# Kernel optimization log

Hardware: AMD Instinct MI355X
Metric: run time of the kernel (lower is better)

Reference implementation:

```python
import jax, jax.numpy as jnp
import numpy as np

N_USERS = 50000
N_ENT = 100000
N_EDGES = 2_000_000
N_INTER = 1_000_000
CHANNEL = 64
N_HEADS = 2
D_K = CHANNEL // N_HEADS
N_HOPS = 2
N_REL = 10  # relation_emb has N_REL-1 rows


def setup_inputs() -> dict:
    key = jax.random.key(0)
    ks = jax.random.split(key, 8)
    user_emb = jax.random.normal(ks[0], (N_USERS, CHANNEL), jnp.float32) * 0.1
    entity_emb = jax.random.normal(ks[1], (N_ENT, CHANNEL), jnp.float32) * 0.1
    relation_emb = jax.random.normal(ks[2], (N_REL - 1, CHANNEL), jnp.float32) * 0.1
    W_Q = jax.random.normal(ks[3], (CHANNEL, CHANNEL), jnp.float32) * (1.0 / np.sqrt(CHANNEL))
    edge_index = jax.random.randint(ks[4], (2, N_EDGES), 0, N_ENT)
    edge_type = jax.random.randint(ks[5], (N_EDGES,), 1, N_REL)  # in [1, N_REL-1]
    inter_edge = jnp.stack([
        jax.random.randint(ks[6], (N_INTER,), 0, N_USERS),
        jax.random.randint(ks[7], (N_INTER,), 0, N_ENT),
    ])
    inter_edge_w = jnp.full((N_INTER,), 1.0 / 20.0, jnp.float32)
    return {
        "user_emb": user_emb,
        "entity_emb": entity_emb,
        "relation_emb": relation_emb,
        "W_Q": W_Q,
        "inter_edge_w": inter_edge_w,
        "edge_index": edge_index,
        "edge_type": edge_type,
        "inter_edge": inter_edge,
    }


def _l2norm(x):
    # F.normalize(dim=-1) with eps=1e-12
    n = jnp.linalg.norm(x, axis=-1, keepdims=True)
    return x / jnp.maximum(n, 1e-12)


def _scatter_softmax(logits, seg, num_segments):
    # per-segment (over leading axis) numerically-stable softmax; logits [E, H]
    m = jax.ops.segment_max(logits, seg, num_segments=num_segments)
    e = jnp.exp(logits - m[seg])
    s = jax.ops.segment_sum(e, seg, num_segments=num_segments)
    return e / s[seg]


def reference(user_emb, entity_emb, relation_emb, W_Q, inter_edge_w,
              edge_index, edge_type, inter_edge):
    head, tail = edge_index[0], edge_index[1]
    u_idx, i_idx = inter_edge[0], inter_edge[1]
    rel = relation_emb[edge_type - 1]  # [E, C]
    inv_sqrt_dk = 1.0 / np.sqrt(D_K)

    entity_res, user_res = entity_emb, user_emb
    for _ in range(N_HOPS):
        h_emb = entity_emb[head]                       # [E, C]
        t_emb = entity_emb[tail]                       # [E, C]
        q = (h_emb @ W_Q).reshape(-1, N_HEADS, D_K)    # [E, H, Dk]
        k = (t_emb @ W_Q).reshape(-1, N_HEADS, D_K) * rel.reshape(-1, N_HEADS, D_K)
        score = (q * k).sum(-1) * inv_sqrt_dk          # [E, H]
        attn = _scatter_softmax(score, head, N_ENT)    # [E, H]
        value = (t_emb * rel).reshape(-1, N_HEADS, D_K)
        agg = (value * attn[..., None]).reshape(-1, CHANNEL)
        entity_agg = jax.ops.segment_sum(agg, head, num_segments=N_ENT)
        item_agg = inter_edge_w[:, None] * entity_emb[i_idx]
        user_agg = jax.ops.segment_sum(item_agg, u_idx, num_segments=N_USERS)
        # mess_dropout disabled (eval mode)
        entity_emb = _l2norm(entity_agg)
        user_emb = _l2norm(user_agg)
        entity_res = entity_res + entity_emb
        user_res = user_res + user_emb
    return entity_res, user_res
```

## Files before the change

### kernel.cpp

```cpp
#include <hip/hip_runtime.h>

#define NU     50000
#define NEN    100000
#define NEDGE  2000000
#define NINTER 1000000
#define CH     64
#define NRELM1 9
#define CAPE   64
#define CAPU   64

#define BINSH   8
#define NBINE   ((NEN + 255) >> BINSH)
#define NBINU   ((NU  + 255) >> BINSH)
#define CHUNKE  8192
#define CHUNKU  4096
#define NBE_BLK ((NEDGE  + CHUNKE - 1) / CHUNKE)
#define NBU_BLK ((NINTER + CHUNKU - 1) / CHUNKU)
#define DSTRE   416
#define DSTRU   224
#define NSTR_E  ((NEN * CH) / 2048)
#define NSTR_U  ((NU * CH + 2047) / 2048)

typedef _Float16 hv2 __attribute__((ext_vector_type(2)));
typedef _Float16 h8  __attribute__((ext_vector_type(8)));
typedef float    f32x4 __attribute__((ext_vector_type(4)));
union P4 { float4 f; hv2 h[4]; };

__global__ __launch_bounds__(256) void k_bin(
    const float* __restrict__ ue, const float* __restrict__ ee,
    const float* __restrict__ re, const float* __restrict__ wq,
    const float* __restrict__ iw, const int* __restrict__ eidx,
    const int* __restrict__ etype, const int* __restrict__ ii,
    _Float16* __restrict__ Eh, float* __restrict__ Eres, float* __restrict__ Ures,
    _Float16* __restrict__ Relh, _Float16* __restrict__ Wt,
    unsigned* __restrict__ dirE, unsigned* __restrict__ dirU,
    int* __restrict__ blkBufE, unsigned long long* __restrict__ blkBufU)
{
    __shared__ long long srt64[CHUNKU];
    __shared__ int hist[512];
    __shared__ int sc[512];
    int* srt = (int*)srt64;
    int b = blockIdx.x, tid = threadIdx.x;

    if (b < NBE_BLK) {
        hist[tid] = 0; hist[tid + 256] = 0;
        __syncthreads();
        int base = b * CHUNKE;
        int n = NEDGE - base; if (n > CHUNKE) n = CHUNKE;
        for (int i = tid; i < n; i += 256)
            atomicAdd(&hist[eidx[base + i] >> BINSH], 1);
        __syncthreads();
        sc[tid] = hist[tid]; sc[tid + 256] = hist[tid + 256];
        __syncthreads();
#pragma unroll
        for (int off = 1; off < 512; off <<= 1) {
            int v0 = (tid >= off) ? sc[tid - off] : 0;
            int v1 = sc[tid + 256 - off];
            __syncthreads();
            sc[tid] += v0; sc[tid + 256] += v1;
            __syncthreads();
        }
        sc[tid] -= hist[tid]; sc[tid + 256] -= hist[tid + 256];
        __syncthreads();
        for (int i = tid; i < n; i += 256) {
            int h  = eidx[base + i];
            int t  = eidx[NEDGE + base + i];
            int rt = etype[base + i] - 1;
            int pos = atomicAdd(&sc[h >> BINSH], 1);
            srt[pos] = (h & 255) | ((t | (rt << 17)) << 8);
        }
        __syncthreads();
        int4* dst = (int4*)(blkBufE + b * CHUNKE);
        const int4* s4 = (const int4*)srt;
        for (int j = tid; j < ((n + 3) >> 2); j += 256) dst[j] = s4[j];
        for (int bin = tid; bin < NBINE; bin += 256)
            dirE[b * DSTRE + bin] =
                ((unsigned)(sc[bin] - hist[bin]) << 16) | (unsigned)hist[bin];
    } else if (b < NBE_BLK + NBU_BLK) {
        hist[tid] = 0; hist[tid + 256] = 0;
        __syncthreads();
        int ub = b - NBE_BLK;
        int base = ub * CHUNKU;
        int n = NINTER - base; if (n > CHUNKU) n = CHUNKU;
        for (int i = tid; i < n; i += 256)
            atomicAdd(&hist[ii[base + i] >> BINSH], 1);
        __syncthreads();
        sc[tid] = hist[tid]; sc[tid + 256] = hist[tid + 256];
        __syncthreads();
#pragma unroll
        for (int off = 1; off < 512; off <<= 1) {
            int v0 = (tid >= off) ? sc[tid - off] : 0;
            int v1 = sc[tid + 256 - off];
            __syncthreads();
            sc[tid] += v0; sc[tid + 256] += v1;
            __syncthreads();
        }
        sc[tid] -= hist[tid]; sc[tid + 256] -= hist[tid + 256];
        __syncthreads();
        for (int i = tid; i < n; i += 256) {
            int u = ii[base + i];
            int e = ii[NINTER + base + i];
            unsigned w = __float_as_uint(iw[base + i]);
            int pos = atomicAdd(&sc[u >> BINSH], 1);
            srt64[pos] = (unsigned long long)((u & 255) | (e << 8))
                       | ((unsigned long long)w << 32);
        }
        __syncthreads();
        int4* dst = (int4*)(blkBufU + (size_t)ub * CHUNKU);
        const int4* s4 = (const int4*)srt64;
        for (int j = tid; j < ((n + 1) >> 1); j += 256) dst[j] = s4[j];
        for (int bin = tid; bin < NBINU; bin += 256)
            dirU[ub * DSTRU + bin] =
                ((unsigned)(sc[bin] - hist[bin]) << 16) | (unsigned)hist[bin];
    } else {
        int sb = b - (NBE_BLK + NBU_BLK);
        if (sb < NSTR_E) {
            int i0 = sb * 2048 + tid * 8;
            float4 a = *(const float4*)(ee + i0);
            float4 c = *(const float4*)(ee + i0 + 4);
            *(float4*)(Eres + i0)     = a;
            *(float4*)(Eres + i0 + 4) = c;
            P4 o;
            o.h[0].x = (_Float16)a.x; o.h[0].y = (_Float16)a.y;
            o.h[1].x = (_Float16)a.z; o.h[1].y = (_Float16)a.w;
            o.h[2].x = (_Float16)c.x; o.h[2].y = (_Float16)c.y;
            o.h[3].x = (_Float16)c.z; o.h[3].y = (_Float16)c.w;
            *(float4*)(Eh + i0) = o.f;
        } else if (sb < NSTR_E + NSTR_U) {
            int i0 = (sb - NSTR_E) * 2048 + tid * 8;
            if (i0 < NU * CH) {
                *(float4*)(Ures + i0)     = *(const float4*)(ue + i0);
                *(float4*)(Ures + i0 + 4) = *(const float4*)(ue + i0 + 4);
            }
        } else {
            for (int i = tid; i < NRELM1 * CH; i += 256)
                Relh[i] = (_Float16)re[i];
            for (int i = tid; i < CH * CH; i += 256)
                Wt[(i & 63) * 64 + (i >> 6)] = (_Float16)wq[i];
        }
    }
}

__global__ __launch_bounds__(256) void k_place(
    const unsigned* __restrict__ dirE, const int* __restrict__ blkBufE,
    const unsigned* __restrict__ dirU, const unsigned long long* __restrict__ blkBufU,
    int* __restrict__ cntE, int* __restrict__ csrE,
    int* __restrict__ cntU, unsigned long long* __restrict__ csrU2)
{
    __shared__ int cnt[256];
    int b = blockIdx.x, tid = threadIdx.x;
    cnt[tid] = 0;
    __syncthreads();
    if (b < NBINE) {
        if (tid < NBE_BLK) {
            unsigned d = dirE[tid * DSTRE + b];
            int off = d >> 16, c = d & 0xFFFF;
            const int* src = blkBufE + tid * CHUNKE + off;
            for (int i = 0; i < c; ++i) {
                int rec = src[i];
                int nl = rec & 255;
                int pos = atomicAdd(&cnt[nl], 1);
                if (pos < CAPE) csrE[((b << BINSH) + nl) * CAPE + pos] = rec >> 8;
            }
        }
        __syncthreads();
        int node = (b << BINSH) + tid;
        if (node < NEN) { int c = cnt[tid]; cntE[node] = c > CAPE ? CAPE : c; }
    } else {
        int ub = b - NBINE;
        if (tid < NBU_BLK) {
            unsigned d = dirU[tid * DSTRU + ub];
            int off = d >> 16, c = d & 0xFFFF;
            const unsigned long long* src = blkBufU + (size_t)tid * CHUNKU + off;
            for (int i = 0; i < c; ++i) {
                unsigned long long rec = src[i];
                int nl = (int)rec & 255;
                int pos = atomicAdd(&cnt[nl], 1);
                if (pos < CAPU)
                    csrU2[((ub << BINSH) + nl) * CAPU + pos] =
                        ((rec & 0xFFFFFFFFull) >> 8) | (rec & 0xFFFFFFFF00000000ull);
            }
        }
        __syncthreads();
        int node = (ub << BINSH) + tid;
        if (node < NU) { int c = cnt[tid]; cntU[node] = c > CAPU ? CAPU : c; }
    }
}

__global__ __launch_bounds__(256) void k_gemm(
    const _Float16* __restrict__ Eh, const _Float16* __restrict__ Wt,
    _Float16* __restrict__ Qh)
{
    int w = threadIdx.x >> 6, lane = threadIdx.x & 63;
    int r0 = blockIdx.x * 64 + w * 16;
    if (r0 >= NEN) return;
    int lr = lane & 15, lg = lane >> 4;
    const _Float16* arow = Eh + (size_t)(r0 + lr) * 64 + lg * 8;
    h8 a0 = *(const h8*)(arow);
    h8 a1 = *(const h8*)(arow + 32);
#pragma unroll
    for (int ct = 0; ct < 4; ++ct) {
        const _Float16* brow = Wt + (ct * 16 + lr) * 64 + lg * 8;
        h8 b0 = *(const h8*)(brow);
        h8 b1 = *(const h8*)(brow + 32);
        f32x4 c = {0.f, 0.f, 0.f, 0.f};
        c = __builtin_amdgcn_mfma_f32_16x16x32_f16(a0, b0, c, 0, 0, 0);
        c = __builtin_amdgcn_mfma_f32_16x16x32_f16(a1, b1, c, 0, 0, 0);
#pragma unroll
        for (int r = 0; r < 4; ++r)
            Qh[(size_t)(r0 + lg * 4 + r) * 64 + ct * 16 + lr] = (_Float16)c[r];
    }
}

__global__ __launch_bounds__(256) void k_fused(
    const int* __restrict__ cntE, const int* __restrict__ csrE,
    const _Float16* __restrict__ Qh, const _Float16* __restrict__ Eh,
    const _Float16* __restrict__ Relh,
    _Float16* __restrict__ Ehn, float* __restrict__ Eres,
    const int* __restrict__ cntU, const unsigned long long* __restrict__ csrU2,
    float* __restrict__ Ures)
{
    int wid  = blockIdx.x * 4 + (threadIdx.x >> 6);
    int lane = threadIdx.x & 63;
    int s = lane >> 3, l = lane & 7;
    int c8 = l * 8;

    if (wid < NEN) {
        int row = wid;
        int cnt = cntE[row];
        int beg = row * CAPE, end = beg + cnt;
        P4 q; q.f = *(const float4*)(Qh + (size_t)row * 64 + c8);
        float acc[8] = {0.f,0.f,0.f,0.f,0.f,0.f,0.f,0.f};
        float den = 0.f;
        int a0 = beg + s;
        int pA = (a0 < end) ? csrE[a0] : 0;
        int pB = (a0 + 8 < end) ? csrE[a0 + 8] : 0;
        P4 ktA, teA, rlA;
        {
            int tail = pA & 0x1FFFF, rt = pA >> 17;
            ktA.f = *(const float4*)(Qh   + (size_t)tail * 64 + c8);
            teA.f = *(const float4*)(Eh   + (size_t)tail * 64 + c8);
            rlA.f = *(const float4*)(Relh + rt * 64 + c8);
        }
        int nit = (cnt + 7) >> 3;
        for (int it = 0; it < nit; ++it) {
            P4 ktB, teB, rlB;
            int tailB = pB & 0x1FFFF, rtB = pB >> 17;
            ktB.f = *(const float4*)(Qh   + (size_t)tailB * 64 + c8);
            teB.f = *(const float4*)(Eh   + (size_t)tailB * 64 + c8);
            rlB.f = *(const float4*)(Relh + rtB * 64 + c8);
            int a2 = beg + (it + 2) * 8 + s;
            int pN = (a2 < end) ? csrE[a2] : 0;
            bool act = (beg + it * 8 + s) < end;
            float sc = 0.f;
#pragma unroll
            for (int i = 0; i < 4; ++i) {
                hv2 km = ktA.h[i] * rlA.h[i];
                sc = __builtin_amdgcn_fdot2(q.h[i], km, sc, false);
            }
            sc += __shfl_xor(sc, 1);
            sc += __shfl_xor(sc, 2);
            float ex = act ? __expf(sc * 0.17677669529663687f) : 0.f;
            den += ex;
#pragma unroll
            for (int i = 0; i < 4; ++i) {
                hv2 vm = teA.h[i] * rlA.h[i];
                acc[2*i]   += ex * (float)vm.x;
                acc[2*i+1] += ex * (float)vm.y;
            }
            ktA = ktB; teA = teB; rlA = rlB; pB = pN;
        }
#pragma unroll
        for (int k = 0; k < 8; ++k) {
            acc[k] += __shfl_xor(acc[k], 8);
            acc[k] += __shfl_xor(acc[k], 16);
            acc[k] += __shfl_xor(acc[k], 32);
        }
        den += __shfl_xor(den, 8); den += __shfl_xor(den, 16); den += __shfl_xor(den, 32);
        float invd = (den > 0.f) ? 1.f / den : 0.f;
        float ss = 0.f;
#pragma unroll
        for (int k = 0; k < 8; ++k) { acc[k] *= invd; ss += acc[k] * acc[k]; }
        ss += __shfl_xor(ss, 1); ss += __shfl_xor(ss, 2); ss += __shfl_xor(ss, 4);
        float inv = 1.f / fmaxf(sqrtf(ss), 1e-12f);
#pragma unroll
        for (int k = 0; k < 8; ++k) acc[k] *= inv;
        if (s == 0) {
            P4 o;
#pragma unroll
            for (int i = 0; i < 4; ++i) { o.h[i].x = (_Float16)acc[2*i]; o.h[i].y = (_Float16)acc[2*i+1]; }
            *(float4*)(Ehn + (size_t)row * 64 + c8) = o.f;
            float4 r0 = *(const float4*)(Eres + (size_t)row * 64 + c8);
            float4 r1 = *(const float4*)(Eres + (size_t)row * 64 + c8 + 4);
            r0.x += acc[0]; r0.y += acc[1]; r0.z += acc[2]; r0.w += acc[3];
            r1.x += acc[4]; r1.y += acc[5]; r1.z += acc[6]; r1.w += acc[7];
            *(float4*)(Eres + (size_t)row * 64 + c8)     = r0;
            *(float4*)(Eres + (size_t)row * 64 + c8 + 4) = r1;
        }
    } else {
        int row = wid - NEN;
        int cnt = cntU[row];
        int beg = row * CAPU, end = beg + cnt;
        float acc[8] = {0.f,0.f,0.f,0.f,0.f,0.f,0.f,0.f};
        int a0 = beg + s;
        unsigned long long recA = (a0 < end) ? csrU2[a0] : 0ull;
        unsigned long long recB = (a0 + 8 < end) ? csrU2[a0 + 8] : 0ull;
        P4 teA; teA.f = *(const float4*)(Eh + (size_t)(unsigned)recA * 64 + c8);
        int nit = (cnt + 7) >> 3;
        for (int it = 0; it < nit; ++it) {
            P4 teB; teB.f = *(const float4*)(Eh + (size_t)(unsigned)recB * 64 + c8);
            int a2 = beg + (it + 2) * 8 + s;
            unsigned long long recN = (a2 < end) ? csrU2[a2] : 0ull;
            float wgt = __uint_as_float((unsigned)(recA >> 32));
#pragma unroll
            for (int i = 0; i < 4; ++i) {
                acc[2*i]   += wgt * (float)teA.h[i].x;
                acc[2*i+1] += wgt * (float)teA.h[i].y;
            }
            teA = teB; recA = recB; recB = recN;
        }
#pragma unroll
        for (int k = 0; k < 8; ++k) {
            acc[k] += __shfl_xor(acc[k], 8);
            acc[k] += __shfl_xor(acc[k], 16);
            acc[k] += __shfl_xor(acc[k], 32);
        }
        float ss = 0.f;
#pragma unroll
        for (int k = 0; k < 8; ++k) ss += acc[k] * acc[k];
        ss += __shfl_xor(ss, 1); ss += __shfl_xor(ss, 2); ss += __shfl_xor(ss, 4);
        float inv = 1.f / fmaxf(sqrtf(ss), 1e-12f);
        if (s == 0) {
            float4 r0 = *(const float4*)(Ures + (size_t)row * 64 + c8);
            float4 r1 = *(const float4*)(Ures + (size_t)row * 64 + c8 + 4);
            r0.x += acc[0] * inv; r0.y += acc[1] * inv; r0.z += acc[2] * inv; r0.w += acc[3] * inv;
            r1.x += acc[4] * inv; r1.y += acc[5] * inv; r1.z += acc[6] * inv; r1.w += acc[7] * inv;
            *(float4*)(Ures + (size_t)row * 64 + c8)     = r0;
            *(float4*)(Ures + (size_t)row * 64 + c8 + 4) = r1;
        }
    }
}

extern "C" void kernel_launch(void* const* d_in, const int* in_sizes, int n_in,
                              void* d_out, int out_size, void* d_ws, size_t ws_size,
                              hipStream_t stream)
{
    const float* ue = (const float*)d_in[0];
    const float* ee = (const float*)d_in[1];
    const float* re = (const float*)d_in[2];
    const float* wq = (const float*)d_in[3];
    const float* iw = (const float*)d_in[4];
    const int* eidx  = (const int*)d_in[5];
    const int* etype = (const int*)d_in[6];
    const int* ii    = (const int*)d_in[7];

    float* Eres = (float*)d_out;
    float* Ures = Eres + (size_t)NEN * CH;

    _Float16* Relh = (_Float16*)d_ws;
    _Float16* Wt   = Relh + 1024;
    _Float16* Qh   = Wt + 4096;
    _Float16* EhA  = Qh  + (size_t)NEN * CH;
    _Float16* EhB  = EhA + (size_t)NEN * CH;
    int* cntE      = (int*)(EhB + (size_t)NEN * CH);
    int* cntU      = cntE + NEN;
    int* csrE      = cntU + NU;
    unsigned long long* csrU2 = (unsigned long long*)(csrE + (size_t)NEN * CAPE);
    unsigned* dirE = (unsigned*)(csrU2 + (size_t)NU * CAPU);
    unsigned* dirU = dirE + NBE_BLK * DSTRE;
    int* blkBufE   = (int*)Qh;
    unsigned long long* blkBufU = (unsigned long long*)EhB;

    k_bin<<<NBE_BLK + NBU_BLK + NSTR_E + NSTR_U + 1, 256, 0, stream>>>(
        ue, ee, re, wq, iw, eidx, etype, ii,
        EhA, Eres, Ures, Relh, Wt, dirE, dirU, blkBufE, blkBufU);
    k_place<<<NBINE + NBINU, 256, 0, stream>>>(dirE, blkBufE, dirU, blkBufU,
                                               cntE, csrE, cntU, csrU2);

    _Float16* Ehc = EhA;
    _Float16* Ehn = EhB;
    for (int hop = 0; hop < 2; ++hop) {
        k_gemm <<<(NEN + 63) / 64, 256, 0, stream>>>(Ehc, Wt, Qh);
        k_fused<<<(NEN + NU) / 4, 256, 0, stream>>>(cntE, csrE, Qh, Ehc, Relh,
                                                    Ehn, Eres, cntU, csrU2, Ures);
        _Float16* tmp = Ehc; Ehc = Ehn; Ehn = tmp;
    }
}
```

Before: 433.7 us.

## Interleave entity embedding and Q projection per node, stage relations in LDS

```diff
diff --git a/kernel.cpp b/kernel.cpp
--- a/kernel.cpp
+++ b/kernel.cpp
@@ -26,12 +26,17 @@
 typedef float    f32x4 __attribute__((ext_vector_type(4)));
 union P4 { float4 f; hv2 h[4]; };
 
+static __device__ __forceinline__ hv2 pkrtz(float a, float b) {
+    return __builtin_bit_cast(hv2, __builtin_amdgcn_cvt_pkrtz(a, b));
+}
+
+
 __global__ __launch_bounds__(256) void k_bin(
     const float* __restrict__ ue, const float* __restrict__ ee,
     const float* __restrict__ re, const float* __restrict__ wq,
     const float* __restrict__ iw, const int* __restrict__ eidx,
     const int* __restrict__ etype, const int* __restrict__ ii,
-    _Float16* __restrict__ Eh, float* __restrict__ Eres, float* __restrict__ Ures,
+    _Float16* __restrict__ QE, float* __restrict__ Eres, float* __restrict__ Ures,
     _Float16* __restrict__ Relh, _Float16* __restrict__ Wt,
     unsigned* __restrict__ dirE, unsigned* __restrict__ dirU,
     int* __restrict__ blkBufE, unsigned long long* __restrict__ blkBufU)
@@ -121,11 +126,12 @@
             *(float4*)(Eres + i0)     = a;
             *(float4*)(Eres + i0 + 4) = c;
             P4 o;
-            o.h[0].x = (_Float16)a.x; o.h[0].y = (_Float16)a.y;
-            o.h[1].x = (_Float16)a.z; o.h[1].y = (_Float16)a.w;
-            o.h[2].x = (_Float16)c.x; o.h[2].y = (_Float16)c.y;
-            o.h[3].x = (_Float16)c.z; o.h[3].y = (_Float16)c.w;
-            *(float4*)(Eh + i0) = o.f;
+            o.h[0] = pkrtz(a.x, a.y);
+            o.h[1] = pkrtz(a.z, a.w);
+            o.h[2] = pkrtz(c.x, c.y);
+            o.h[3] = pkrtz(c.z, c.w);
+            int node = i0 >> 6, c0 = i0 & 63;
+            *(float4*)(QE + (size_t)node * 128 + c0) = o.f;
         } else if (sb < NSTR_E + NSTR_U) {
             int i0 = (sb - NSTR_E) * 2048 + tid * 8;
             if (i0 < NU * CH) {
@@ -188,14 +194,13 @@
 }
 
 __global__ __launch_bounds__(256) void k_gemm(
-    const _Float16* __restrict__ Eh, const _Float16* __restrict__ Wt,
-    _Float16* __restrict__ Qh)
+    _Float16* __restrict__ QE, const _Float16* __restrict__ Wt)
 {
     int w = threadIdx.x >> 6, lane = threadIdx.x & 63;
     int r0 = blockIdx.x * 64 + w * 16;
     if (r0 >= NEN) return;
     int lr = lane & 15, lg = lane >> 4;
-    const _Float16* arow = Eh + (size_t)(r0 + lr) * 64 + lg * 8;
+    const _Float16* arow = QE + (size_t)(r0 + lr) * 128 + lg * 8;
     h8 a0 = *(const h8*)(arow);
     h8 a1 = *(const h8*)(arow + 32);
 #pragma unroll
@@ -208,20 +213,24 @@
         c = __builtin_amdgcn_mfma_f32_16x16x32_f16(a1, b1, c, 0, 0, 0);
 #pragma unroll
         for (int r = 0; r < 4; ++r)
-            Qh[(size_t)(r0 + lg * 4 + r) * 64 + ct * 16 + lr] = (_Float16)c[r];
+            QE[(size_t)(r0 + lg * 4 + r) * 128 + 64 + ct * 16 + lr] = (_Float16)c[r];
     }
 }
 
 __global__ __launch_bounds__(256) void k_fused(
     const int* __restrict__ cntE, const int* __restrict__ csrE,
-    const _Float16* __restrict__ Qh, const _Float16* __restrict__ Eh,
-    const _Float16* __restrict__ Relh,
-    _Float16* __restrict__ Ehn, float* __restrict__ Eres,
+    const _Float16* __restrict__ QE, const _Float16* __restrict__ Relh,
+    _Float16* __restrict__ QEn, float* __restrict__ Eres,
     const int* __restrict__ cntU, const unsigned long long* __restrict__ csrU2,
     float* __restrict__ Ures)
 {
-    int wid  = blockIdx.x * 4 + (threadIdx.x >> 6);
-    int lane = threadIdx.x & 63;
+    __shared__ __attribute__((aligned(16))) _Float16 RelL[NRELM1 * 64];
+    int tid = threadIdx.x;
+    if (tid < 72) *(float4*)(RelL + tid * 8) = *(const float4*)(Relh + tid * 8);
+    __syncthreads();
+
+    int wid  = blockIdx.x * 4 + (tid >> 6);
+    int lane = tid & 63;
     int s = lane >> 3, l = lane & 7;
     int c8 = l * 8;
 
@@ -229,71 +238,94 @@
         int row = wid;
         int cnt = cntE[row];
         int beg = row * CAPE, end = beg + cnt;
-        P4 q; q.f = *(const float4*)(Qh + (size_t)row * 64 + c8);
+        P4 q; q.f = *(const float4*)(QE + (size_t)row * 128 + 64 + c8);
         float acc[8] = {0.f,0.f,0.f,0.f,0.f,0.f,0.f,0.f};
         float den = 0.f;
-        int a0 = beg + s;
-        int pA = (a0 < end) ? csrE[a0] : 0;
-        int pB = (a0 + 8 < end) ? csrE[a0 + 8] : 0;
-        P4 ktA, teA, rlA;
-        {
-            int tail = pA & 0x1FFFF, rt = pA >> 17;
-            ktA.f = *(const float4*)(Qh   + (size_t)tail * 64 + c8);
-            teA.f = *(const float4*)(Eh   + (size_t)tail * 64 + c8);
-            rlA.f = *(const float4*)(Relh + rt * 64 + c8);
-        }
-        int nit = (cnt + 7) >> 3;
-        for (int it = 0; it < nit; ++it) {
-            P4 ktB, teB, rlB;
-            int tailB = pB & 0x1FFFF, rtB = pB >> 17;
-            ktB.f = *(const float4*)(Qh   + (size_t)tailB * 64 + c8);
-            teB.f = *(const float4*)(Eh   + (size_t)tailB * 64 + c8);
-            rlB.f = *(const float4*)(Relh + rtB * 64 + c8);
-            int a2 = beg + (it + 2) * 8 + s;
-            int pN = (a2 < end) ? csrE[a2] : 0;
-            bool act = (beg + it * 8 + s) < end;
+
+        auto compute = [&](const P4& te, const P4& kt, const P4& rl, bool act) {
             float sc = 0.f;
 #pragma unroll
             for (int i = 0; i < 4; ++i) {
-                hv2 km = ktA.h[i] * rlA.h[i];
+                hv2 km = kt.h[i] * rl.h[i];
                 sc = __builtin_amdgcn_fdot2(q.h[i], km, sc, false);
             }
             sc += __shfl_xor(sc, 1);
             sc += __shfl_xor(sc, 2);
-            float ex = act ? __expf(sc * 0.17677669529663687f) : 0.f;
+            float ex = exp2f(sc * 0.25503489f);
+            if (!act) ex = 0.f;
             den += ex;
 #pragma unroll
             for (int i = 0; i < 4; ++i) {
-                hv2 vm = teA.h[i] * rlA.h[i];
+                hv2 vm = te.h[i] * rl.h[i];
                 acc[2*i]   += ex * (float)vm.x;
                 acc[2*i+1] += ex * (float)vm.y;
             }
-            ktA = ktB; teA = teB; rlA = rlB; pB = pN;
-        }
-#pragma unroll
-        for (int k = 0; k < 8; ++k) {
-            acc[k] += __shfl_xor(acc[k], 8);
-            acc[k] += __shfl_xor(acc[k], 16);
-            acc[k] += __shfl_xor(acc[k], 32);
-        }
-        den += __shfl_xor(den, 8); den += __shfl_xor(den, 16); den += __shfl_xor(den, 32);
+        };
+
+        int p0 = beg + s;
+        int iA = (p0 < end) ? csrE[p0] : 0;
+        int iB = (p0 + 8 < end) ? csrE[p0 + 8] : 0;
+        P4 teA, ktA, rlA;
+        {
+            const _Float16* bA = QE + (size_t)(iA & 0x1FFFF) * 128 + c8;
+            teA.f = *(const float4*)bA;
+            ktA.f = *(const float4*)(bA + 64);
+            rlA.f = *(const float4*)(RelL + (iA >> 17) * 64 + c8);
+        }
+        for (int p = p0; p < end; p += 16) {
+            P4 teB, ktB, rlB;
+            {
+                const _Float16* bB = QE + (size_t)(iB & 0x1FFFF) * 128 + c8;
+                teB.f = *(const float4*)bB;
+                ktB.f = *(const float4*)(bB + 64);
+                rlB.f = *(const float4*)(RelL + (iB >> 17) * 64 + c8);
+            }
+            int iC = (p + 16 < end) ? csrE[p + 16] : 0;
+            compute(teA, ktA, rlA, true);
+            {
+                const _Float16* bC = QE + (size_t)(iC & 0x1FFFF) * 128 + c8;
+                teA.f = *(const float4*)bC;
+                ktA.f = *(const float4*)(bC + 64);
+                rlA.f = *(const float4*)(RelL + (iC >> 17) * 64 + c8);
+            }
+            int iD = (p + 24 < end) ? csrE[p + 24] : 0;
+            compute(teB, ktB, rlB, p + 8 < end);
+            iB = iD;
+        }
+        hv2 pk[4];
+#pragma unroll
+        for (int i = 0; i < 4; ++i)
+            pk[i] = pkrtz(acc[2*i], acc[2*i+1]);
+#pragma unroll
+        for (int m = 8; m <= 32; m <<= 1) {
+#pragma unroll
+            for (int i = 0; i < 4; ++i) {
+                int v = __shfl_xor(__builtin_bit_cast(int, pk[i]), m);
+                pk[i] += __builtin_bit_cast(hv2, v);
+            }
+            den += __shfl_xor(den, m);
+        }
+        float af[8];
+#pragma unroll
+        for (int i = 0; i < 4; ++i) { af[2*i] = (float)pk[i].x; af[2*i+1] = (float)pk[i].y; }
         float invd = (den > 0.f) ? 1.f / den : 0.f;
         float ss = 0.f;
 #pragma unroll
-        for (int k = 0; k < 8; ++k) { acc[k] *= invd; ss += acc[k] * acc[k]; }
+        for (int k = 0; k < 8; ++k) { af[k] *= invd; ss += af[k] * af[k]; }
         ss += __shfl_xor(ss, 1); ss += __shfl_xor(ss, 2); ss += __shfl_xor(ss, 4);
         float inv = 1.f / fmaxf(sqrtf(ss), 1e-12f);
 #pragma unroll
-        for (int k = 0; k < 8; ++k) acc[k] *= inv;
+        for (int k = 0; k < 8; ++k) af[k] *= inv;
         if (s == 0) {
             P4 o;
 #pragma unroll
-            for (int i = 0; i < 4; ++i) { o.h[i].x = (_Float16)acc[2*i]; o.h[i].y = (_Float16)acc[2*i+1]; }
-            *(float4*)(Ehn + (size_t)row * 64 + c8) = o.f;
+            for (int i = 0; i < 4; ++i)
+                o.h[i] = pkrtz(af[2*i], af[2*i+1]);
+            *(float4*)(QEn + (size_t)row * 128 + c8) = o.f;
             float4 r0 = *(const float4*)(Eres + (size_t)row * 64 + c8);
             float4 r1 = *(const float4*)(Eres + (size_t)row * 64 + c8 + 4);
-            r0.x += acc[0]; r0.y += acc[1]; r0.z += acc[2]; r0.w += acc[3];
-            r1.x += acc[4]; r1.y += acc[5]; r1.z += acc[6]; r1.w += acc[7];
+            r0.x += af[0]; r0.y += af[1]; r0.z += af[2]; r0.w += af[3];
+            r1.x += af[4]; r1.y += af[5]; r1.z += af[6]; r1.w += af[7];
             *(float4*)(Eres + (size_t)row * 64 + c8)     = r0;
             *(float4*)(Eres + (size_t)row * 64 + c8 + 4) = r1;
         }
@@ -302,39 +334,54 @@
         int cnt = cntU[row];
         int beg = row * CAPU, end = beg + cnt;
         float acc[8] = {0.f,0.f,0.f,0.f,0.f,0.f,0.f,0.f};
-        int a0 = beg + s;
-        unsigned long long recA = (a0 < end) ? csrU2[a0] : 0ull;
-        unsigned long long recB = (a0 + 8 < end) ? csrU2[a0 + 8] : 0ull;
-        P4 teA; teA.f = *(const float4*)(Eh + (size_t)(unsigned)recA * 64 + c8);
-        int nit = (cnt + 7) >> 3;
-        for (int it = 0; it < nit; ++it) {
-            P4 teB; teB.f = *(const float4*)(Eh + (size_t)(unsigned)recB * 64 + c8);
-            int a2 = beg + (it + 2) * 8 + s;
-            unsigned long long recN = (a2 < end) ? csrU2[a2] : 0ull;
-            float wgt = __uint_as_float((unsigned)(recA >> 32));
-#pragma unroll
-            for (int i = 0; i < 4; ++i) {
-                acc[2*i]   += wgt * (float)teA.h[i].x;
-                acc[2*i+1] += wgt * (float)teA.h[i].y;
-            }
-            teA = teB; recA = recB; recB = recN;
-        }
-#pragma unroll
-        for (int k = 0; k < 8; ++k) {
-            acc[k] += __shfl_xor(acc[k], 8);
-            acc[k] += __shfl_xor(acc[k], 16);
-            acc[k] += __shfl_xor(acc[k], 32);
-        }
+        int p0 = beg + s;
+        unsigned long long recA = (p0 < end) ? csrU2[p0] : 0ull;
+        unsigned long long recB = (p0 + 8 < end) ? csrU2[p0 + 8] : 0ull;
+        P4 teA; teA.f = *(const float4*)(QE + (size_t)(unsigned)recA * 128 + c8);
+        for (int p = p0; p < end; p += 16) {
+            P4 teB; teB.f = *(const float4*)(QE + (size_t)(unsigned)recB * 128 + c8);
+            unsigned long long recC = (p + 16 < end) ? csrU2[p + 16] : 0ull;
+            float wA = __uint_as_float((unsigned)(recA >> 32));
+#pragma unroll
+            for (int i = 0; i < 4; ++i) {
+                acc[2*i]   += wA * (float)teA.h[i].x;
+                acc[2*i+1] += wA * (float)teA.h[i].y;
+            }
+            teA.f = *(const float4*)(QE + (size_t)(unsigned)recC * 128 + c8);
+            unsigned long long recD = (p + 24 < end) ? csrU2[p + 24] : 0ull;
+            float wB = __uint_as_float((unsigned)(recB >> 32));
+#pragma unroll
+            for (int i = 0; i < 4; ++i) {
+                acc[2*i]   += wB * (float)teB.h[i].x;
+                acc[2*i+1] += wB * (float)teB.h[i].y;
+            }
+            recA = recC; recB = recD;
+        }
+        hv2 pk[4];
+#pragma unroll
+        for (int i = 0; i < 4; ++i)
+            pk[i] = pkrtz(acc[2*i], acc[2*i+1]);
+#pragma unroll
+        for (int m = 8; m <= 32; m <<= 1) {
+#pragma unroll
+            for (int i = 0; i < 4; ++i) {
+                int v = __shfl_xor(__builtin_bit_cast(int, pk[i]), m);
+                pk[i] += __builtin_bit_cast(hv2, v);
+            }
+        }
+        float af[8];
+#pragma unroll
+        for (int i = 0; i < 4; ++i) { af[2*i] = (float)pk[i].x; af[2*i+1] = (float)pk[i].y; }
         float ss = 0.f;
 #pragma unroll
-        for (int k = 0; k < 8; ++k) ss += acc[k] * acc[k];
+        for (int k = 0; k < 8; ++k) ss += af[k] * af[k];
         ss += __shfl_xor(ss, 1); ss += __shfl_xor(ss, 2); ss += __shfl_xor(ss, 4);
         float inv = 1.f / fmaxf(sqrtf(ss), 1e-12f);
         if (s == 0) {
             float4 r0 = *(const float4*)(Ures + (size_t)row * 64 + c8);
             float4 r1 = *(const float4*)(Ures + (size_t)row * 64 + c8 + 4);
-            r0.x += acc[0] * inv; r0.y += acc[1] * inv; r0.z += acc[2] * inv; r0.w += acc[3] * inv;
-            r1.x += acc[4] * inv; r1.y += acc[5] * inv; r1.z += acc[6] * inv; r1.w += acc[7] * inv;
+            r0.x += af[0] * inv; r0.y += af[1] * inv; r0.z += af[2] * inv; r0.w += af[3] * inv;
+            r1.x += af[4] * inv; r1.y += af[5] * inv; r1.z += af[6] * inv; r1.w += af[7] * inv;
             *(float4*)(Ures + (size_t)row * 64 + c8)     = r0;
             *(float4*)(Ures + (size_t)row * 64 + c8 + 4) = r1;
         }
@@ -359,30 +406,30 @@
 
     _Float16* Relh = (_Float16*)d_ws;
     _Float16* Wt   = Relh + 1024;
-    _Float16* Qh   = Wt + 4096;
-    _Float16* EhA  = Qh  + (size_t)NEN * CH;
-    _Float16* EhB  = EhA + (size_t)NEN * CH;
-    int* cntE      = (int*)(EhB + (size_t)NEN * CH);
+    _Float16* QEA  = Wt + 4096;
+    _Float16* QEB  = QEA + (size_t)NEN * 128;
+    int* cntE      = (int*)(QEB + (size_t)NEN * 128);
     int* cntU      = cntE + NEN;
     int* csrE      = cntU + NU;
     unsigned long long* csrU2 = (unsigned long long*)(csrE + (size_t)NEN * CAPE);
     unsigned* dirE = (unsigned*)(csrU2 + (size_t)NU * CAPU);
     unsigned* dirU = dirE + NBE_BLK * DSTRE;
-    int* blkBufE   = (int*)Qh;
-    unsigned long long* blkBufU = (unsigned long long*)EhB;
+    int* blkBufE   = (int*)QEB;
+    unsigned long long* blkBufU =
+        (unsigned long long*)((char*)QEB + (size_t)NBE_BLK * CHUNKE * 4);
 
     k_bin<<<NBE_BLK + NBU_BLK + NSTR_E + NSTR_U + 1, 256, 0, stream>>>(
         ue, ee, re, wq, iw, eidx, etype, ii,
-        EhA, Eres, Ures, Relh, Wt, dirE, dirU, blkBufE, blkBufU);
+        QEA, Eres, Ures, Relh, Wt, dirE, dirU, blkBufE, blkBufU);
     k_place<<<NBINE + NBINU, 256, 0, stream>>>(dirE, blkBufE, dirU, blkBufU,
                                                cntE, csrE, cntU, csrU2);
 
-    _Float16* Ehc = EhA;
-    _Float16* Ehn = EhB;
+    _Float16* QEc = QEA;
+    _Float16* QEn = QEB;
     for (int hop = 0; hop < 2; ++hop) {
-        k_gemm <<<(NEN + 63) / 64, 256, 0, stream>>>(Ehc, Wt, Qh);
-        k_fused<<<(NEN + NU) / 4, 256, 0, stream>>>(cntE, csrE, Qh, Ehc, Relh,
-                                                    Ehn, Eres, cntU, csrU2, Ures);
-        _Float16* tmp = Ehc; Ehc = Ehn; Ehn = tmp;
+        k_gemm <<<(NEN + 63) / 64, 256, 0, stream>>>(QEc, Wt);
+        k_fused<<<(NEN + NU) / 4, 256, 0, stream>>>(cntE, csrE, QEc, Relh,
+                                                    QEn, Eres, cntU, csrU2, Ures);
+        _Float16* tmp = QEc; QEc = QEn; QEn = tmp;
     }
 }
```

Measured after the change: 448.2 us. +3.3%, slower.
